# Optimization experiments

Measured on AMD Instinct MI355X. Metric: run time of the kernel, lower is better.

## Reference

```python
import jax, jax.numpy as jnp
import numpy as np

B, S, D, H = 2, 2048, 1024, 16
HD = D // H

def setup_inputs() -> dict:
    key = jax.random.key(0)
    ks = jax.random.split(key, 9)
    s = 1.0 / np.sqrt(D)
    return {
        "x": jax.random.normal(ks[0], (B, S, D), jnp.float32),
        "Wq": jax.random.uniform(ks[1], (D, D), jnp.float32, -s, s),
        "bq": jax.random.uniform(ks[2], (D,), jnp.float32, -s, s),
        "Wk": jax.random.uniform(ks[3], (D, D), jnp.float32, -s, s),
        "bk": jax.random.uniform(ks[4], (D,), jnp.float32, -s, s),
        "Wv": jax.random.uniform(ks[5], (D, D), jnp.float32, -s, s),
        "bv": jax.random.uniform(ks[6], (D,), jnp.float32, -s, s),
        "Wo": jax.random.uniform(ks[7], (D, D), jnp.float32, -s, s),
        "bo": jax.random.uniform(ks[8], (D,), jnp.float32, -s, s),
    }

def reference(x, Wq, bq, Wk, bk, Wv, bv, Wo, bo):
    b, s, _ = x.shape
    # projections (torch Linear: y = x @ W.T + b; here W stored as [in,out])
    q = x @ Wq + bq
    k = x @ Wk + bk
    v = x @ Wv + bv
    # [b, h, s, hd]
    q = q.reshape(b, s, H, HD).transpose(0, 2, 1, 3)
    k = k.reshape(b, s, H, HD).transpose(0, 2, 1, 3)
    v = v.reshape(b, s, H, HD).transpose(0, 2, 1, 3)
    scores = jnp.einsum("bhqd,bhkd->bhqk", q, k) / jnp.sqrt(jnp.float32(HD))
    weights = jax.nn.softmax(scores, axis=-1)
    attn = jnp.einsum("bhqk,bhkd->bhqd", weights, v)
    attn = attn.transpose(0, 2, 1, 3).reshape(b, s, D)
    return attn @ Wo + bo
```

## Files before the change

kernel.cpp:

```cpp
#include <hip/hip_runtime.h>
#include <hip/hip_bf16.h>
#include <stdint.h>

#define B_  2
#define S_  2048
#define D_  1024
#define H_  16
#define HD_ 64
#define M_  (B_*S_)

typedef __attribute__((ext_vector_type(8)))  short short8;
typedef __attribute__((ext_vector_type(4)))  float f32x4;
typedef __attribute__((ext_vector_type(16))) float f32x16;

__device__ __forceinline__ unsigned short f2bf(float f) {
  union { float f; unsigned int u; } x; x.f = f;
  unsigned int r = (x.u + 0x7FFFu + ((x.u >> 16) & 1u)) >> 16;
  return (unsigned short)r;
}

__device__ __forceinline__ unsigned int pack2(float a, float b) {
  union { float f; unsigned int u; } x, y; x.f = a; y.f = b;
  return __builtin_amdgcn_perm(y.u + 0x8000u, x.u + 0x8000u, 0x07060302u);
}

typedef const __attribute__((address_space(1))) unsigned int* gas1_t;
typedef __attribute__((address_space(3))) unsigned int* las3_t;

__device__ __forceinline__ void gload_lds16(const void* g, void* l) {
  __builtin_amdgcn_global_load_lds((gas1_t)g, (las3_t)l, 16, 0, 0);
}

__global__ void k_cvt_bf16(const float* __restrict__ x, ushort* __restrict__ o, int n4) {
  int i = blockIdx.x * blockDim.x + threadIdx.x;
  int stride = gridDim.x * blockDim.x;
  for (int j = i; j < n4; j += stride) {
    float4 v = ((const float4*)x)[j];
    ushort4 u = make_ushort4(f2bf(v.x), f2bf(v.y), f2bf(v.z), f2bf(v.w));
    ((ushort4*)o)[j] = u;
  }
}

__global__ void k_transpose_w(const float* __restrict__ w0, const float* __restrict__ w1,
                              const float* __restrict__ w2, const float* __restrict__ w3,
                              ushort* __restrict__ o0, ushort* __restrict__ o1,
                              ushort* __restrict__ o2, ushort* __restrict__ o3) {
  const float* w = (blockIdx.z == 0) ? w0 : (blockIdx.z == 1) ? w1 : (blockIdx.z == 2) ? w2 : w3;
  ushort*      o = (blockIdx.z == 0) ? o0 : (blockIdx.z == 1) ? o1 : (blockIdx.z == 2) ? o2 : o3;
  __shared__ float t[32][33];
  int tx = threadIdx.x & 31, ty = threadIdx.x >> 5;
  int kt = blockIdx.y * 32, nt = blockIdx.x * 32;
  #pragma unroll
  for (int i = 0; i < 4; ++i)
    t[ty + 8 * i][tx] = w[(size_t)(kt + ty + 8 * i) * D_ + nt + tx];
  __syncthreads();
  #pragma unroll
  for (int i = 0; i < 4; ++i)
    o[(size_t)(nt + ty + 8 * i) * D_ + kt + tx] = f2bf(t[tx][ty + 8 * i]);
}

__global__ __launch_bounds__(256) void k_gemm_bt(const ushort* __restrict__ A,
                                                 const ushort* __restrict__ Bt,
                                                 const float* __restrict__ b0,
                                                 const float* __restrict__ b1,
                                                 const float* __restrict__ b2,
                                                 void* __restrict__ o0,
                                                 void* __restrict__ o1,
                                                 void* __restrict__ o2, int mode) {
  __shared__ char smem[2][32768];
  const int tid = threadIdx.x;
  const int w = tid >> 6, lane = tid & 63;
  const int g = lane >> 4, c = lane & 15;
  const int m0 = blockIdx.y * 128, n0 = blockIdx.x * 128;
  const int wm = (w >> 1) * 64, wn = (w & 1) * 64;

  f32x4 acc[4][4];
  #pragma unroll
  for (int i = 0; i < 4; ++i)
    #pragma unroll
    for (int j = 0; j < 4; ++j) acc[i][j] = 0.f;

  const char* Abase = (const char*)A + (size_t)m0 * (D_ * 2);
  const char* Bbase = (const char*)Bt + (size_t)n0 * (D_ * 2);

  auto stage = [&](int buf, int kb) {
    char* ls = &smem[buf][0];
    #pragma unroll
    for (int i = 0; i < 4; ++i) {
      int obase = w * 4096 + i * 1024;
      int ot = obase + lane * 16;
      int u = ot ^ (((ot >> 7) & 7) << 4);
      gload_lds16(Abase + (size_t)(u >> 7) * (D_ * 2) + kb * 128 + (u & 127), ls + obase);
    }
    #pragma unroll
    for (int i = 0; i < 4; ++i) {
      int obase = w * 4096 + i * 1024;
      int ot = obase + lane * 16;
      int u = ot ^ (((ot >> 7) & 7) << 4);
      gload_lds16(Bbase + (size_t)(u >> 7) * (D_ * 2) + kb * 128 + (u & 127), ls + 16384 + obase);
    }
  };

  stage(0, 0);
  int cur = 0;
  for (int kb = 0; kb < D_ / 64; ++kb) {
    __syncthreads();
    if (kb < D_ / 64 - 1) stage(cur ^ 1, kb + 1);
    const char* lsA = &smem[cur][0];
    const char* lsB = lsA + 16384;
    short8 a[4][2], b[4][2];
    #pragma unroll
    for (int f = 0; f < 4; ++f) {
      int rowA = wm + f * 16 + c;
      int rowB = wn + f * 16 + c;
      #pragma unroll
      for (int ks = 0; ks < 2; ++ks) {
        int offA = (rowA * 128 + ks * 64 + g * 16) ^ ((rowA & 7) << 4);
        int offB = (rowB * 128 + ks * 64 + g * 16) ^ ((rowB & 7) << 4);
        a[f][ks] = *(const short8*)(lsA + offA);
        b[f][ks] = *(const short8*)(lsB + offB);
      }
    }
    #pragma unroll
    for (int mf = 0; mf < 4; ++mf)
      #pragma unroll
      for (int nf = 0; nf < 4; ++nf) {
        acc[mf][nf] = __builtin_amdgcn_mfma_f32_16x16x32_bf16(a[mf][0], b[nf][0], acc[mf][nf], 0, 0, 0);
        acc[mf][nf] = __builtin_amdgcn_mfma_f32_16x16x32_bf16(a[mf][1], b[nf][1], acc[mf][nf], 0, 0, 0);
      }
    cur ^= 1;
  }

  const int sec = n0 >> 10;
  const float* bb = (mode == 1) ? b0 : (sec == 0) ? b0 : (sec == 1) ? b1 : b2;
  void* outp = (mode == 1) ? o0 : (sec == 0) ? o0 : (sec == 1) ? o1 : o2;
  #pragma unroll
  for (int nf = 0; nf < 4; ++nf) {
    int col = n0 + wn + nf * 16 + c;
    int lc = col & 1023;
    float bvv = bb[lc];
    #pragma unroll
    for (int mf = 0; mf < 4; ++mf) {
      #pragma unroll
      for (int r = 0; r < 4; ++r) {
        int tok = m0 + wm + mf * 16 + 4 * g + r;
        float v = acc[mf][nf][r] + bvv;
        if (mode == 1) {
          ((float*)outp)[(size_t)tok * D_ + col] = v;
        } else {
          if (sec == 0) v *= 0.18033688011112042f;
          int bi = tok >> 11, si = tok & 2047;
          int h = lc >> 6, hd = lc & 63;
          size_t off = (sec == 2)
            ? ((size_t)(bi * H_ + h) * HD_ + hd) * S_ + si
            : ((size_t)(bi * H_ + h) * S_ + si) * HD_ + hd;
          ((ushort*)outp)[off] = f2bf(v);
        }
      }
    }
  }
}

__global__ __launch_bounds__(256, 2) void k_attn(const ushort* __restrict__ Q,
                                                 const ushort* __restrict__ K,
                                                 const ushort* __restrict__ Vt,
                                                 ushort* __restrict__ O) {
  __shared__ char lds[2][16384];
  const int tid = threadIdx.x;
  const int w = tid >> 6, lane = tid & 63;
  const int ql = lane & 31, hi = lane >> 5;
  const int bid = blockIdx.x;
  const int bh = (bid & 7) * 4 + ((bid >> 3) & 3);
  const int qc = bid >> 5;
  const int q0 = qc * 128 + w * 32;
  const ushort* Qb = Q + (size_t)bh * S_ * HD_;
  const char* Kb2 = (const char*)(K + (size_t)bh * S_ * HD_);
  const char* Vb2 = (const char*)(Vt + (size_t)bh * HD_ * S_);

  short8 qf[4];
  #pragma unroll
  for (int t = 0; t < 4; ++t)
    qf[t] = *(const short8*)(Qb + (size_t)(q0 + ql) * HD_ + 16 * t + 8 * hi);

  short8 vones;
  #pragma unroll
  for (int i = 0; i < 8; ++i) vones[i] = (short)0x3F80;

  auto stageKV = [&](int buf, int k0n) {
    char* ls = &lds[buf][0];
    #pragma unroll
    for (int i = 0; i < 2; ++i) {
      int o = tid * 16 + i * 4096;
      int u = o ^ (((o >> 7) & 7) << 4);
      gload_lds16(Kb2 + (size_t)(k0n + (u >> 7)) * 128 + (u & 127), ls + o);
    }
    #pragma unroll
    for (int i = 0; i < 2; ++i) {
      int o = tid * 16 + i * 4096;
      int u = o ^ (((o >> 7) & 7) << 4);
      gload_lds16(Vb2 + (size_t)(u >> 7) * (S_ * 2) + (size_t)k0n * 2 + (u & 127), ls + 8192 + o);
    }
  };

  f32x16 oacc[2], lacc;
  oacc[0] = 0.f; oacc[1] = 0.f; lacc = 0.f;
  float m = -1e30f;

  stageKV(0, 0);
  int cur = 0;
  for (int k0 = 0; k0 < S_; k0 += 64) {
    __syncthreads();
    if (k0 + 64 < S_) stageKV(cur ^ 1, k0 + 64);
    const char* lsK = &lds[cur][0];
    const char* lsV = lsK + 8192;

    f32x16 st[2];
    #pragma unroll
    for (int n = 0; n < 2; ++n) {
      st[n] = 0.f;
      #pragma unroll
      for (int t = 0; t < 4; ++t) {
        int row = 32 * n + ql, col = 32 * t + 16 * hi;
        short8 kf = *(const short8*)(lsK + ((row * 128 + col) ^ ((row & 7) << 4)));
        st[n] = __builtin_amdgcn_mfma_f32_32x32x16_bf16(kf, qf[t], st[n], 0, 0, 0);
      }
    }

    float red[16];
    #pragma unroll
    for (int i = 0; i < 16; ++i) red[i] = fmaxf(st[0][i], st[1][i]);
    #pragma unroll
    for (int s = 8; s >= 1; s >>= 1)
      #pragma unroll
      for (int i = 0; i < s; ++i) red[i] = fmaxf(red[i], red[i + s]);
    float cmax = fmaxf(red[0], __shfl_xor(red[0], 32));

    if (!__all(cmax - m <= 8.0f)) {
      float mnew = fmaxf(m, cmax);
      float sc = exp2f(m - mnew);
      m = mnew;
      #pragma unroll
      for (int i = 0; i < 16; ++i) { oacc[0][i] *= sc; oacc[1][i] *= sc; }
      lacc[0] *= sc;
    }

    short8 pfrag[2][2];
    #pragma unroll
    for (int n = 0; n < 2; ++n) {
      unsigned int pk[4][2];
      #pragma unroll
      for (int b = 0; b < 4; ++b)
        #pragma unroll
        for (int p = 0; p < 2; ++p)
          pk[b][p] = pack2(exp2f(st[n][4 * b + 2 * p] - m), exp2f(st[n][4 * b + 2 * p + 1] - m));
      #pragma unroll
      for (int m2 = 0; m2 < 2; ++m2) {
        union { unsigned int u[4]; short8 v; } fr;
        fr.u[0] = pk[2 * m2][0];     fr.u[1] = pk[2 * m2][1];
        fr.u[2] = pk[2 * m2 + 1][0]; fr.u[3] = pk[2 * m2 + 1][1];
        pfrag[n][m2] = fr.v;
      }
    }

    #pragma unroll
    for (int n = 0; n < 2; ++n)
      #pragma unroll
      for (int m2 = 0; m2 < 2; ++m2)
        lacc = __builtin_amdgcn_mfma_f32_32x32x16_bf16(vones, pfrag[n][m2], lacc, 0, 0, 0);

    #pragma unroll
    for (int dt = 0; dt < 2; ++dt) {
      const int rb = (32 * dt + ql) * 128;
      const int sz = (ql & 7) << 4;
      #pragma unroll
      for (int n = 0; n < 2; ++n)
        #pragma unroll
        for (int m2 = 0; m2 < 2; ++m2) {
          const int cb = 64 * n + 32 * m2 + 8 * hi;
          union { struct { unsigned long long a, b; } q; short8 v; } vf;
          vf.q.a = *(const unsigned long long*)(lsV + ((rb + cb) ^ sz));
          vf.q.b = *(const unsigned long long*)(lsV + ((rb + cb + 16) ^ sz));
          oacc[dt] = __builtin_amdgcn_mfma_f32_32x32x16_bf16(vf.v, pfrag[n][m2], oacc[dt], 0, 0, 0);
        }
    }
    cur ^= 1;
  }

  const float invl = 1.f / lacc[0];
  const int bi = bh >> 4, h = bh & 15;
  const int tok = bi * S_ + q0 + ql;
  #pragma unroll
  for (int dt = 0; dt < 2; ++dt)
    #pragma unroll
    for (int rg = 0; rg < 4; ++rg) {
      ushort4 u;
      u.x = f2bf(oacc[dt][4 * rg + 0] * invl);
      u.y = f2bf(oacc[dt][4 * rg + 1] * invl);
      u.z = f2bf(oacc[dt][4 * rg + 2] * invl);
      u.w = f2bf(oacc[dt][4 * rg + 3] * invl);
      *(ushort4*)(O + (size_t)tok * D_ + h * 64 + dt * 32 + rg * 8 + 4 * hi) = u;
    }
}

extern "C" void kernel_launch(void* const* d_in, const int* in_sizes, int n_in,
                              void* d_out, int out_size, void* d_ws, size_t ws_size,
                              hipStream_t stream) {
  const float* x  = (const float*)d_in[0];
  const float* Wq = (const float*)d_in[1];
  const float* bq = (const float*)d_in[2];
  const float* Wk = (const float*)d_in[3];
  const float* bk = (const float*)d_in[4];
  const float* Wv = (const float*)d_in[5];
  const float* bv = (const float*)d_in[6];
  const float* Wo = (const float*)d_in[7];
  const float* bo = (const float*)d_in[8];
  char* ws = (char*)d_ws;
  const size_t MB = 1024 * 1024;
  ushort* Xbf = (ushort*)(ws + 0);
  ushort* Wt3 = (ushort*)(ws + 8 * MB);
  ushort* Wto = (ushort*)(ws + 14 * MB);
  ushort* Qb  = (ushort*)(ws + 16 * MB);
  ushort* Kb  = (ushort*)(ws + 24 * MB);
  ushort* Vtb = (ushort*)(ws + 32 * MB);
  ushort* Att = (ushort*)(ws + 0);

  k_cvt_bf16<<<1024, 256, 0, stream>>>(x, Xbf, M_ * D_ / 4);
  k_transpose_w<<<dim3(32, 32, 4), 256, 0, stream>>>(
      Wq, Wk, Wv, Wo, Wt3, Wt3 + 1024 * 1024, Wt3 + 2048 * 1024, Wto);
  k_gemm_bt<<<dim3(24, 32), 256, 0, stream>>>(Xbf, Wt3, bq, bk, bv, Qb, Kb, Vtb, 0);
  k_attn<<<512, 256, 0, stream>>>(Qb, Kb, Vtb, Att);
  k_gemm_bt<<<dim3(8, 32), 256, 0, stream>>>(Att, Wto, bo, bo, bo, d_out, d_out, d_out, 1);
}
```

Baseline: 226.3 us.

## Split attention key range across two wave groups and merge partial softmax

Doubles the attention block to 512 threads, with two groups of four waves each processing half of the key sequence for the same 128 queries (split-K flash attention within a block). Each group stages its own K/V tiles in a separate LDS region. At the end, group 1 writes its partial output, max and sum to LDS and group 0 rescales and merges them before writing bf16. This raises waves per CU and halves the serial key loop per wave, to hide latency better on 512 blocks, at the cost of double the LDS and a merge step.

After: 256.9 us. +13.5%, slower.

```diff
diff --git a/kernel.cpp b/kernel.cpp
--- a/kernel.cpp
+++ b/kernel.cpp
@@ -161,18 +161,21 @@
   }
 }
 
-__global__ __launch_bounds__(256, 2) void k_attn(const ushort* __restrict__ Q,
+__global__ __launch_bounds__(512, 4) void k_attn(const ushort* __restrict__ Q,
                                                  const ushort* __restrict__ K,
                                                  const ushort* __restrict__ Vt,
                                                  ushort* __restrict__ O) {
-  __shared__ char lds[2][16384];
+  __shared__ __align__(16) char lds[2][2][16384];
   const int tid = threadIdx.x;
   const int w = tid >> 6, lane = tid & 63;
+  const int qw = w & 3, g2 = w >> 2;
+  const int tl = tid & 255;
   const int ql = lane & 31, hi = lane >> 5;
   const int bid = blockIdx.x;
   const int bh = (bid & 7) * 4 + ((bid >> 3) & 3);
   const int qc = bid >> 5;
-  const int q0 = qc * 128 + w * 32;
+  const int q0 = qc * 128 + qw * 32;
+  const int kbase = g2 * 1024;
   const ushort* Qb = Q + (size_t)bh * S_ * HD_;
   const char* Kb2 = (const char*)(K + (size_t)bh * S_ * HD_);
   const char* Vb2 = (const char*)(Vt + (size_t)bh * HD_ * S_);
@@ -187,16 +190,16 @@
   for (int i = 0; i < 8; ++i) vones[i] = (short)0x3F80;
 
   auto stageKV = [&](int buf, int k0n) {
-    char* ls = &lds[buf][0];
+    char* ls = &lds[buf][g2][0];
     #pragma unroll
     for (int i = 0; i < 2; ++i) {
-      int o = tid * 16 + i * 4096;
+      int o = tl * 16 + i * 4096;
       int u = o ^ (((o >> 7) & 7) << 4);
       gload_lds16(Kb2 + (size_t)(k0n + (u >> 7)) * 128 + (u & 127), ls + o);
     }
     #pragma unroll
     for (int i = 0; i < 2; ++i) {
-      int o = tid * 16 + i * 4096;
+      int o = tl * 16 + i * 4096;
       int u = o ^ (((o >> 7) & 7) << 4);
       gload_lds16(Vb2 + (size_t)(u >> 7) * (S_ * 2) + (size_t)k0n * 2 + (u & 127), ls + 8192 + o);
     }
@@ -206,12 +209,12 @@
   oacc[0] = 0.f; oacc[1] = 0.f; lacc = 0.f;
   float m = -1e30f;
 
-  stageKV(0, 0);
+  stageKV(0, kbase);
   int cur = 0;
-  for (int k0 = 0; k0 < S_; k0 += 64) {
+  for (int kk = 0; kk < 16; ++kk) {
     __syncthreads();
-    if (k0 + 64 < S_) stageKV(cur ^ 1, k0 + 64);
-    const char* lsK = &lds[cur][0];
+    if (kk < 15) stageKV(cur ^ 1, kbase + (kk + 1) * 64);
+    const char* lsK = &lds[cur][g2][0];
     const char* lsV = lsK + 8192;
 
     f32x16 st[2];
@@ -286,20 +289,48 @@
     cur ^= 1;
   }
 
-  const float invl = 1.f / lacc[0];
-  const int bi = bh >> 4, h = bh & 15;
-  const int tok = bi * S_ + q0 + ql;
-  #pragma unroll
-  for (int dt = 0; dt < 2; ++dt)
-    #pragma unroll
-    for (int rg = 0; rg < 4; ++rg) {
-      ushort4 u;
-      u.x = f2bf(oacc[dt][4 * rg + 0] * invl);
-      u.y = f2bf(oacc[dt][4 * rg + 1] * invl);
-      u.z = f2bf(oacc[dt][4 * rg + 2] * invl);
-      u.w = f2bf(oacc[dt][4 * rg + 3] * invl);
-      *(ushort4*)(O + (size_t)tok * D_ + h * 64 + dt * 32 + rg * 8 + 4 * hi) = u;
-    }
+  float l = lacc[0];
+  __syncthreads();
+  float* fl = (float*)&lds[0][0][0];
+  if (g2 == 1) {
+    float* ob = fl + (qw * 32 + ql) * 64;
+    #pragma unroll
+    for (int dt = 0; dt < 2; ++dt)
+      #pragma unroll
+      for (int rg = 0; rg < 4; ++rg) {
+        f32x4 v;
+        v[0] = oacc[dt][4 * rg + 0]; v[1] = oacc[dt][4 * rg + 1];
+        v[2] = oacc[dt][4 * rg + 2]; v[3] = oacc[dt][4 * rg + 3];
+        *(f32x4*)(ob + dt * 32 + rg * 8 + 4 * hi) = v;
+      }
+    if (hi == 0) {
+      fl[8192 + (qw * 32 + ql) * 2 + 0] = m;
+      fl[8192 + (qw * 32 + ql) * 2 + 1] = l;
+    }
+  }
+  __syncthreads();
+  if (g2 == 0) {
+    float mp = fl[8192 + (qw * 32 + ql) * 2 + 0];
+    float lp = fl[8192 + (qw * 32 + ql) * 2 + 1];
+    float mm = fmaxf(m, mp);
+    float a  = exp2f(m - mm), ap = exp2f(mp - mm);
+    float invl = 1.f / (l * a + lp * ap);
+    const float* ob = fl + (qw * 32 + ql) * 64;
+    const int bi = bh >> 4, h = bh & 15;
+    const int tok = bi * S_ + q0 + ql;
+    #pragma unroll
+    for (int dt = 0; dt < 2; ++dt)
+      #pragma unroll
+      for (int rg = 0; rg < 4; ++rg) {
+        f32x4 pv = *(const f32x4*)(ob + dt * 32 + rg * 8 + 4 * hi);
+        ushort4 u;
+        u.x = f2bf((oacc[dt][4 * rg + 0] * a + pv[0] * ap) * invl);
+        u.y = f2bf((oacc[dt][4 * rg + 1] * a + pv[1] * ap) * invl);
+        u.z = f2bf((oacc[dt][4 * rg + 2] * a + pv[2] * ap) * invl);
+        u.w = f2bf((oacc[dt][4 * rg + 3] * a + pv[3] * ap) * invl);
+        *(ushort4*)(O + (size_t)tok * D_ + h * 64 + dt * 32 + rg * 8 + 4 * hi) = u;
+      }
+  }
 }
 
 extern "C" void kernel_launch(void* const* d_in, const int* in_sizes, int n_in,
@@ -328,6 +359,6 @@
   k_transpose_w<<<dim3(32, 32, 4), 256, 0, stream>>>(
       Wq, Wk, Wv, Wo, Wt3, Wt3 + 1024 * 1024, Wt3 + 2048 * 1024, Wto);
   k_gemm_bt<<<dim3(24, 32), 256, 0, stream>>>(Xbf, Wt3, bq, bk, bv, Qb, Kb, Vtb, 0);
-  k_attn<<<512, 256, 0, stream>>>(Qb, Kb, Vtb, Att);
+  k_attn<<<512, 512, 0, stream>>>(Qb, Kb, Vtb, Att);
   k_gemm_bt<<<dim3(8, 32), 256, 0, stream>>>(Att, Wto, bo, bo, bo, d_out, d_out, d_out, 1);
 }
```
